# Kernel optimization log

Hardware: AMD Instinct MI355X
Metric: run time of the kernel (lower is better)

## Reference

```python
import jax, jax.numpy as jnp
import numpy as np

B = 8192
IN = 1024
H = 1024


def setup_inputs() -> dict:
    key = jax.random.key(0)
    ks = jax.random.split(key, 12)
    def xavier(k, shape):
        fan_in, fan_out = shape[1], shape[0]
        std = (2.0 / (fan_in + fan_out)) ** 0.5
        return jax.random.normal(k, shape, dtype=jnp.float32) * std
    return {
        "x": jax.random.normal(ks[0], (B, IN), dtype=jnp.float32),
        "hprev": jax.random.normal(ks[1], (B, H), dtype=jnp.float32),
        "c": jax.random.normal(ks[2], (B, 2 * H), dtype=jnp.float32),
        "Wh": xavier(ks[3], (H, IN)),
        "Wz": xavier(ks[4], (H, IN)),
        "Wr": xavier(ks[5], (H, IN)),
        "Uh": xavier(ks[6], (H, H)),
        "Uz": xavier(ks[7], (H, H)),
        "Ur": xavier(ks[8], (H, H)),
        "Ch": xavier(ks[9], (H, 2 * H)),
        "Cz": xavier(ks[10], (H, 2 * H)),
        "Cr": xavier(ks[11], (H, 2 * H)),
        "bh": jnp.zeros((H,), dtype=jnp.float32),
        "bz": jnp.zeros((H,), dtype=jnp.float32),
        "br": jnp.zeros((H,), dtype=jnp.float32),
    }


def reference(x, hprev, c, Wh, Wz, Wr, Uh, Uz, Ur, Ch, Cz, Cr, bh, bz, br):
    # batch_mul(W, v) == v @ W.T for batched vectors
    r = jax.nn.sigmoid(x @ Wr.T + hprev @ Ur.T + c @ Cr.T + br)
    z = jax.nn.sigmoid(x @ Wz.T + hprev @ Uz.T + c @ Cz.T + bz)
    h_prop = jnp.tanh(x @ Wh.T + (r * hprev) @ Uh.T + c @ Ch.T + bh)
    return z * h_prop + (1.0 - z) * hprev
```

## Files before the change

kernel.cpp:

```cpp
#include <hip/hip_runtime.h>
#include <hip/hip_bf16.h>

typedef __attribute__((ext_vector_type(8))) short bf16x8;
typedef __attribute__((ext_vector_type(8))) unsigned short u16x8;
typedef __attribute__((ext_vector_type(4))) float f32x4;

#define BM 128
#define BN 128
#define BK 64

__device__ __forceinline__ unsigned short f2b(float f) {
    union { float f; unsigned int u; } x; x.f = f;
    unsigned int r = x.u + 0x7fffu + ((x.u >> 16) & 1u);
    return (unsigned short)(r >> 16);
}

__device__ __forceinline__ float sigmoidf_(float v) {
    return 1.0f / (1.0f + __expf(-v));
}
__device__ __forceinline__ float tanhf_(float v) {
    return 1.0f - 2.0f / (__expf(2.0f * v) + 1.0f);
}

__device__ __forceinline__ void gll16(const void* g, void* l) {
    __builtin_amdgcn_global_load_lds(
        (const __attribute__((address_space(1))) void*)g,
        (__attribute__((address_space(3))) void*)l,
        16, 0, 0);
}

__device__ __forceinline__ void mma_core(
    const unsigned short* __restrict__ A, int lda,
    const unsigned short* __restrict__ B, int ldb,
    int m0, int n0, int nk, int remap_from, int remap_add,
    unsigned short* As, unsigned short* Bs, f32x4 acc[4][4])
{
    const int t = threadIdx.x;
    const int lane = t & 63;
    const int wm = (t >> 7) & 1;
    const int wn = (t >> 6) & 1;
    const int srow = t >> 3;
    const int ldsCol = (t & 7) * 8;
    const int swc = (((t & 7) ^ ((t >> 3) & 7))) * 8;

    for (int kt = 0; kt < nk; ++kt) {
        int k0 = kt * BK + (kt >= remap_from ? remap_add : 0);
        __syncthreads();
        #pragma unroll
        for (int j = 0; j < 4; ++j) {
            int row = j * 32 + srow;
            gll16(A + (size_t)(m0 + row) * lda + k0 + swc, As + row * BK + ldsCol);
            gll16(B + (size_t)(n0 + row) * ldb + k0 + swc, Bs + row * BK + ldsCol);
        }
        __syncthreads();
        #pragma unroll
        for (int kk = 0; kk < 2; ++kk) {
            bf16x8 af[4], bfr[4];
            const int off = (((kk * 4 + (lane >> 4)) ^ (lane & 7))) * 8;
            const int ra = (wm * 64 + (lane & 15)) * BK + off;
            const int rb = (wn * 64 + (lane & 15)) * BK + off;
            #pragma unroll
            for (int i = 0; i < 4; ++i)
                af[i] = *(const bf16x8*)(As + ra + i * 16 * BK);
            #pragma unroll
            for (int j = 0; j < 4; ++j)
                bfr[j] = *(const bf16x8*)(Bs + rb + j * 16 * BK);
            #pragma unroll
            for (int i = 0; i < 4; ++i)
                #pragma unroll
                for (int j = 0; j < 4; ++j)
                    acc[i][j] = __builtin_amdgcn_mfma_f32_16x16x32_bf16(
                        af[i], bfr[j], acc[i][j], 0, 0, 0);
        }
    }
}

__global__ __launch_bounds__(256, 3) void gemm1(
    const unsigned short* __restrict__ Xall,
    const unsigned short* __restrict__ Wcat,
    const float* __restrict__ hprev,
    const float* __restrict__ br, const float* __restrict__ bz,
    unsigned short* __restrict__ rh,
    float* __restrict__ zout,
    float* __restrict__ shp)
{
    __shared__ __attribute__((aligned(16))) unsigned short As[BM * BK];
    __shared__ __attribute__((aligned(16))) unsigned short Bs[BN * BK];
    f32x4 acc[4][4] = {};

    const int flat = blockIdx.y * gridDim.x + blockIdx.x;
    const int xcd = flat & 7;
    const int p = flat >> 3;
    const int bm = (xcd >> 1) * 16 + (p & 15);
    const int bn = (p >> 4) * 2 + (xcd & 1);

    const int gate = (bn * BN) >> 10;
    const int m0 = bm * BM, n0 = bn * BN;
    const int nk = (gate == 2) ? 48 : 64;
    const int rfrom = (gate == 2) ? 16 : (1 << 30);

    mma_core(Xall, 4096, Wcat, 4096, m0, n0, nk, rfrom, 1024, As, Bs, acc);

    const int lane = threadIdx.x & 63;
    const int wm = (threadIdx.x >> 7) & 1, wn = (threadIdx.x >> 6) & 1;
    const int rowb = m0 + wm * 64 + (lane >> 4) * 4;
    const int colb = (n0 - gate * 1024) + wn * 64 + (lane & 15);

    if (gate == 0) {
        #pragma unroll
        for (int i = 0; i < 4; ++i)
            #pragma unroll
            for (int r = 0; r < 4; ++r) {
                int m = rowb + i * 16 + r;
                #pragma unroll
                for (int j = 0; j < 4; ++j) {
                    int n = colb + j * 16;
                    size_t idx = (size_t)m * 1024 + n;
                    float rr = sigmoidf_(acc[i][j][r] + br[n]);
                    rh[idx] = f2b(rr * hprev[idx]);
                }
            }
    } else if (gate == 1) {
        #pragma unroll
        for (int i = 0; i < 4; ++i)
            #pragma unroll
            for (int r = 0; r < 4; ++r) {
                int m = rowb + i * 16 + r;
                #pragma unroll
                for (int j = 0; j < 4; ++j) {
                    int n = colb + j * 16;
                    size_t idx = (size_t)m * 1024 + n;
                    zout[idx] = sigmoidf_(acc[i][j][r] + bz[n]);
                }
            }
    } else {
        #pragma unroll
        for (int i = 0; i < 4; ++i)
            #pragma unroll
            for (int r = 0; r < 4; ++r) {
                int m = rowb + i * 16 + r;
                #pragma unroll
                for (int j = 0; j < 4; ++j) {
                    int n = colb + j * 16;
                    size_t idx = (size_t)m * 1024 + n;
                    shp[idx] = acc[i][j][r];
                }
            }
    }
}

__global__ __launch_bounds__(256, 3) void gemm2(
    const unsigned short* __restrict__ rh,
    const unsigned short* __restrict__ Uhb,
    const float* __restrict__ shp, const float* __restrict__ bh,
    const float* __restrict__ hprev,
    float* __restrict__ zo)
{
    __shared__ __attribute__((aligned(16))) unsigned short As[BM * BK];
    __shared__ __attribute__((aligned(16))) unsigned short Bs[BN * BK];
    f32x4 acc[4][4] = {};

    const int flat = blockIdx.y * gridDim.x + blockIdx.x;
    const int xcd = flat & 7;
    const int p = flat >> 3;
    const int bm = xcd * 8 + (p & 7);
    const int bn = p >> 3;
    const int m0 = bm * BM, n0 = bn * BN;

    mma_core(rh, 1024, Uhb, 1024, m0, n0, 16, 1 << 30, 0, As, Bs, acc);

    const int lane = threadIdx.x & 63;
    const int wm = (threadIdx.x >> 7) & 1, wn = (threadIdx.x >> 6) & 1;
    const int rowb = m0 + wm * 64 + (lane >> 4) * 4;
    const int colb = n0 + wn * 64 + (lane & 15);

    #pragma unroll
    for (int i = 0; i < 4; ++i)
        #pragma unroll
        for (int r = 0; r < 4; ++r) {
            int m = rowb + i * 16 + r;
            #pragma unroll
            for (int j = 0; j < 4; ++j) {
                int n = colb + j * 16;
                size_t idx = (size_t)m * 1024 + n;
                float val = acc[i][j][r] + shp[idx] + bh[n];
                float hp = tanhf_(val);
                float zv = zo[idx];
                zo[idx] = zv * hp + (1.0f - zv) * hprev[idx];
            }
        }
}

struct CastJobs {
    const float* src[12];
    unsigned short* dst[12];
    int n8[12];
    int cs3[12];
    int stride[12];
};

__global__ __launch_bounds__(256) void cast_all(CastJobs jb) {
    const int job = blockIdx.y;
    const float4* src = (const float4*)jb.src[job];
    unsigned short* dst = jb.dst[job];
    const int n8 = jb.n8[job];
    const int cs3 = jb.cs3[job];
    const int stride = jb.stride[job];
    const int cmask = (1 << cs3) - 1;
    for (int i = blockIdx.x * blockDim.x + threadIdx.x; i < n8;
         i += gridDim.x * blockDim.x) {
        float4 a = src[2 * i];
        float4 b = src[2 * i + 1];
        int row = i >> cs3;
        int col = (i & cmask) * 8;
        u16x8 o;
        o[0] = f2b(a.x); o[1] = f2b(a.y); o[2] = f2b(a.z); o[3] = f2b(a.w);
        o[4] = f2b(b.x); o[5] = f2b(b.y); o[6] = f2b(b.z); o[7] = f2b(b.w);
        *(u16x8*)(dst + (size_t)row * stride + col) = o;
    }
}

extern "C" void kernel_launch(void* const* d_in, const int* in_sizes, int n_in,
                              void* d_out, int out_size, void* d_ws, size_t ws_size,
                              hipStream_t stream) {
    const float* x     = (const float*)d_in[0];
    const float* hprev = (const float*)d_in[1];
    const float* c     = (const float*)d_in[2];
    const float* Wh    = (const float*)d_in[3];
    const float* Wz    = (const float*)d_in[4];
    const float* Wr    = (const float*)d_in[5];
    const float* Uh    = (const float*)d_in[6];
    const float* Uz    = (const float*)d_in[7];
    const float* Ur    = (const float*)d_in[8];
    const float* Ch    = (const float*)d_in[9];
    const float* Cz    = (const float*)d_in[10];
    const float* Cr    = (const float*)d_in[11];
    const float* bh    = (const float*)d_in[12];
    const float* bz    = (const float*)d_in[13];
    const float* br    = (const float*)d_in[14];

    char* ws = (char*)d_ws;
    unsigned short* Xall = (unsigned short*)ws; ws += (size_t)8192 * 4096 * 2;
    unsigned short* Wcat = (unsigned short*)ws; ws += (size_t)3072 * 4096 * 2;
    unsigned short* Uhb  = (unsigned short*)ws; ws += (size_t)1024 * 1024 * 2;
    unsigned short* rhb  = (unsigned short*)ws; ws += (size_t)8192 * 1024 * 2;
    float* shp           = (float*)ws;          ws += (size_t)8192 * 1024 * 4;
    float* zo = (float*)d_out;

    CastJobs jb;
    auto setjob = [&](int j, const float* s, unsigned short* dbase, int col0,
                      int rows, int cols, int stride) {
        jb.src[j] = s; jb.dst[j] = dbase + col0;
        jb.n8[j] = rows * cols / 8;
        jb.cs3[j] = (cols == 2048) ? 8 : 7;
        jb.stride[j] = stride;
    };
    setjob(0, x,     Xall, 0,    8192, 1024, 4096);
    setjob(1, hprev, Xall, 1024, 8192, 1024, 4096);
    setjob(2, c,     Xall, 2048, 8192, 2048, 4096);
    setjob(3, Wr, Wcat, 0,    1024, 1024, 4096);
    setjob(4, Ur, Wcat, 1024, 1024, 1024, 4096);
    setjob(5, Cr, Wcat, 2048, 1024, 2048, 4096);
    setjob(6, Wz, Wcat + 1024 * 4096, 0,    1024, 1024, 4096);
    setjob(7, Uz, Wcat + 1024 * 4096, 1024, 1024, 1024, 4096);
    setjob(8, Cz, Wcat + 1024 * 4096, 2048, 1024, 2048, 4096);
    setjob(9,  Wh, Wcat + 2048 * 4096, 0,    1024, 1024, 4096);
    setjob(10, Ch, Wcat + 2048 * 4096, 2048, 1024, 2048, 4096);
    setjob(11, Uh, Uhb, 0, 1024, 1024, 1024);

    hipLaunchKernelGGL(cast_all, dim3(2048, 12), dim3(256), 0, stream, jb);
    hipLaunchKernelGGL(gemm1, dim3(24, 64), dim3(256), 0, stream,
                       Xall, Wcat, hprev, br, bz, rhb, zo, shp);
    hipLaunchKernelGGL(gemm2, dim3(8, 64), dim3(256), 0, stream,
                       rhb, Uhb, shp, bh, hprev, zo);
}
```

Before: 438.9 us.

## Store gate intermediates in bf16, flatten cast grid, raise occupancy bound

The z gate and the partial h pre-activation are now stored as bf16 intermediates instead of fp32, which halves the bytes written by gemm1 and read by gemm2. The cast kernel moves from a 2D per-job grid to one flat grid that finds each element's job with a prefix search, so load balances across jobs of different sizes. Launch bounds go from 3 to 4 waves per SIMD. The bf16 intermediates cost some precision, and the tighter bound may force register spills.

```diff
diff --git a/kernel.cpp b/kernel.cpp
--- a/kernel.cpp
+++ b/kernel.cpp
@@ -13,6 +13,10 @@
     union { float f; unsigned int u; } x; x.f = f;
     unsigned int r = x.u + 0x7fffu + ((x.u >> 16) & 1u);
     return (unsigned short)(r >> 16);
+}
+__device__ __forceinline__ float b2f(unsigned short b) {
+    union { unsigned int u; float f; } x; x.u = ((unsigned int)b) << 16;
+    return x.f;
 }
 
 __device__ __forceinline__ float sigmoidf_(float v) {
@@ -75,14 +79,14 @@
     }
 }
 
-__global__ __launch_bounds__(256, 3) void gemm1(
+__global__ __launch_bounds__(256, 4) void gemm1(
     const unsigned short* __restrict__ Xall,
     const unsigned short* __restrict__ Wcat,
     const float* __restrict__ hprev,
     const float* __restrict__ br, const float* __restrict__ bz,
     unsigned short* __restrict__ rh,
-    float* __restrict__ zout,
-    float* __restrict__ shp)
+    unsigned short* __restrict__ zs,
+    unsigned short* __restrict__ shp)
 {
     __shared__ __attribute__((aligned(16))) unsigned short As[BM * BK];
     __shared__ __attribute__((aligned(16))) unsigned short Bs[BN * BK];
@@ -130,7 +134,7 @@
                 for (int j = 0; j < 4; ++j) {
                     int n = colb + j * 16;
                     size_t idx = (size_t)m * 1024 + n;
-                    zout[idx] = sigmoidf_(acc[i][j][r] + bz[n]);
+                    zs[idx] = f2b(sigmoidf_(acc[i][j][r] + bz[n]));
                 }
             }
     } else {
@@ -143,18 +147,19 @@
                 for (int j = 0; j < 4; ++j) {
                     int n = colb + j * 16;
                     size_t idx = (size_t)m * 1024 + n;
-                    shp[idx] = acc[i][j][r];
+                    shp[idx] = f2b(acc[i][j][r]);
                 }
             }
     }
 }
 
-__global__ __launch_bounds__(256, 3) void gemm2(
+__global__ __launch_bounds__(256, 4) void gemm2(
     const unsigned short* __restrict__ rh,
     const unsigned short* __restrict__ Uhb,
-    const float* __restrict__ shp, const float* __restrict__ bh,
+    const unsigned short* __restrict__ shp, const float* __restrict__ bh,
+    const unsigned short* __restrict__ zs,
     const float* __restrict__ hprev,
-    float* __restrict__ zo)
+    float* __restrict__ out)
 {
     __shared__ __attribute__((aligned(16))) unsigned short As[BM * BK];
     __shared__ __attribute__((aligned(16))) unsigned short Bs[BN * BK];
@@ -183,10 +188,10 @@
             for (int j = 0; j < 4; ++j) {
                 int n = colb + j * 16;
                 size_t idx = (size_t)m * 1024 + n;
-                float val = acc[i][j][r] + shp[idx] + bh[n];
+                float val = acc[i][j][r] + b2f(shp[idx]) + bh[n];
                 float hp = tanhf_(val);
-                float zv = zo[idx];
-                zo[idx] = zv * hp + (1.0f - zv) * hprev[idx];
+                float zv = b2f(zs[idx]);
+                out[idx] = zv * hp + (1.0f - zv) * hprev[idx];
             }
         }
 }
@@ -194,29 +199,28 @@
 struct CastJobs {
     const float* src[12];
     unsigned short* dst[12];
-    int n8[12];
+    int start[13];
     int cs3[12];
     int stride[12];
 };
 
-__global__ __launch_bounds__(256) void cast_all(CastJobs jb) {
-    const int job = blockIdx.y;
-    const float4* src = (const float4*)jb.src[job];
-    unsigned short* dst = jb.dst[job];
-    const int n8 = jb.n8[job];
-    const int cs3 = jb.cs3[job];
-    const int stride = jb.stride[job];
-    const int cmask = (1 << cs3) - 1;
-    for (int i = blockIdx.x * blockDim.x + threadIdx.x; i < n8;
+__global__ __launch_bounds__(256) void cast_all(CastJobs jb, int total) {
+    for (int i = blockIdx.x * blockDim.x + threadIdx.x; i < total;
          i += gridDim.x * blockDim.x) {
-        float4 a = src[2 * i];
-        float4 b = src[2 * i + 1];
-        int row = i >> cs3;
-        int col = (i & cmask) * 8;
+        int j = 0;
+        #pragma unroll
+        for (int k = 1; k < 12; ++k) j += (i >= jb.start[k]) ? 1 : 0;
+        const int li = i - jb.start[j];
+        const float4* src = (const float4*)jb.src[j];
+        float4 a = src[2 * li];
+        float4 b = src[2 * li + 1];
+        const int cs3 = jb.cs3[j];
+        int row = li >> cs3;
+        int col = (li & ((1 << cs3) - 1)) * 8;
         u16x8 o;
         o[0] = f2b(a.x); o[1] = f2b(a.y); o[2] = f2b(a.z); o[3] = f2b(a.w);
         o[4] = f2b(b.x); o[5] = f2b(b.y); o[6] = f2b(b.z); o[7] = f2b(b.w);
-        *(u16x8*)(dst + (size_t)row * stride + col) = o;
+        *(u16x8*)(jb.dst[j] + (size_t)row * jb.stride[j] + col) = o;
     }
 }
 
@@ -244,14 +248,16 @@
     unsigned short* Wcat = (unsigned short*)ws; ws += (size_t)3072 * 4096 * 2;
     unsigned short* Uhb  = (unsigned short*)ws; ws += (size_t)1024 * 1024 * 2;
     unsigned short* rhb  = (unsigned short*)ws; ws += (size_t)8192 * 1024 * 2;
-    float* shp           = (float*)ws;          ws += (size_t)8192 * 1024 * 4;
-    float* zo = (float*)d_out;
+    unsigned short* shp  = (unsigned short*)ws; ws += (size_t)8192 * 1024 * 2;
+    unsigned short* zsb  = (unsigned short*)ws; ws += (size_t)8192 * 1024 * 2;
 
     CastJobs jb;
+    int acc = 0;
     auto setjob = [&](int j, const float* s, unsigned short* dbase, int col0,
                       int rows, int cols, int stride) {
         jb.src[j] = s; jb.dst[j] = dbase + col0;
-        jb.n8[j] = rows * cols / 8;
+        jb.start[j] = acc;
+        acc += rows * cols / 8;
         jb.cs3[j] = (cols == 2048) ? 8 : 7;
         jb.stride[j] = stride;
     };
@@ -267,10 +273,11 @@
     setjob(9,  Wh, Wcat + 2048 * 4096, 0,    1024, 1024, 4096);
     setjob(10, Ch, Wcat + 2048 * 4096, 2048, 1024, 2048, 4096);
     setjob(11, Uh, Uhb, 0, 1024, 1024, 1024);
-
-    hipLaunchKernelGGL(cast_all, dim3(2048, 12), dim3(256), 0, stream, jb);
+    jb.start[12] = acc;
+
+    hipLaunchKernelGGL(cast_all, dim3(2048), dim3(256), 0, stream, jb, acc);
     hipLaunchKernelGGL(gemm1, dim3(24, 64), dim3(256), 0, stream,
-                       Xall, Wcat, hprev, br, bz, rhb, zo, shp);
+                       Xall, Wcat, hprev, br, bz, rhb, zsb, shp);
     hipLaunchKernelGGL(gemm2, dim3(8, 64), dim3(256), 0, stream,
-                       rhb, Uhb, shp, bh, hprev, zo);
-}
+                       rhb, Uhb, shp, bh, zsb, hprev, (float*)d_out);
+}
```

After: 435.4 us. About the same (-0.8%).
